# Kernel tuning notes

Hardware: AMD Instinct MI355X
Metric: run time of the kernel (lower is better)

Reference implementation:

```python
import jax, jax.numpy as jnp
import numpy as np

B, T, D = 256, 128, 64
H, A, O = 512, 128, 32


def setup_inputs() -> dict:
    key = jax.random.key(0)
    ks = jax.random.split(key, 16)
    u = lambda k, sh, lo, hi: jax.random.uniform(k, sh, jnp.float32, lo, hi)
    return {
        "x_states": jax.random.normal(ks[0], (B, T, D), jnp.float32),
        "x_dts": jax.random.uniform(ks[1], (B, T), jnp.float32) * 0.1,
        # StepwiseAttention params (stored [in, out])
        "Wq": u(ks[2], (D, A), -0.1, 0.1), "bq": u(ks[3], (A,), -0.1, 0.1),
        "Wk": u(ks[4], (H, A), -0.1, 0.1), "bk": u(ks[5], (A,), -0.1, 0.1),
        "Wv": u(ks[6], (H, A), -0.1, 0.1), "bv": u(ks[7], (A,), -0.1, 0.1),
        # LTCAttentionCell params
        "W_gd": u(ks[8], (D + H + A, 2 * H), -0.1, 0.1),
        "b_gd": u(ks[9], (2 * H,), -0.1, 0.1),
        "W_tau": u(ks[10], (H, H), -0.1, 0.1),
        "b_tau": u(ks[11], (H,), -0.1, 0.1),
        "gleak": u(ks[12], (H,), 0.001, 1.0),
        "cm": u(ks[13], (H,), 0.4, 0.6),
        # output head
        "W_fc": u(ks[14], (H, O), -0.1, 0.1),
        "b_fc": u(ks[15], (O,), -0.1, 0.1),
    }


def _forward(x_states, x_dts, Wq, bq, Wk, bk, Wv, bv,
             W_gd, b_gd, W_tau, b_tau, gleak, cm, W_fc, b_fc):
    scale = jnp.sqrt(jnp.asarray(A, jnp.float32))
    leak = jax.nn.softplus(cm) + jax.nn.softplus(gleak)  # [H]

    def dhdt(h, x_t, ctx):
        combined = jnp.concatenate([x_t, h, ctx], axis=1)        # [B, D+H+A]
        gd = combined @ W_gd + b_gd                              # [B, 2H]
        gate, dyn = jnp.split(gd, 2, axis=1)
        tau = jax.nn.softplus(h @ W_tau + b_tau)                 # [B, H]
        num = jax.nn.sigmoid(gate) * jnp.tanh(dyn) - h
        return num / (tau + leak + 1e-6)

    def step(carry, inp):
        h, hist = carry            # h [B,H], hist [B,T,H]
        t, x_t, dt = inp           # t scalar, x_t [B,D], dt [B]
        # stepwise attention over history h_1..h_t
        Q = x_t @ Wq + bq                                        # [B, A]
        K = hist @ Wk + bk                                       # [B, T, A]
        V = hist @ Wv + bv                                       # [B, T, A]
        scores = jnp.einsum('ba,bta->bt', Q, K) / scale          # [B, T]
        valid = jnp.arange(T) < t
        scores = jnp.where(valid[None, :], scores, -1e9)
        w = jax.nn.softmax(scores, axis=-1)
        ctx = jnp.einsum('bt,bta->ba', w, V)
        ctx = jnp.where(t > 0, ctx, jnp.zeros_like(ctx))         # empty history -> 0
        # one RK4 step (torchdiffeq 'rk4' = 3/8-rule variant), step size dt per sample
        dtc = dt[:, None]
        k1 = dhdt(h, x_t, ctx)
        k2 = dhdt(h + dtc * k1 / 3.0, x_t, ctx)
        k3 = dhdt(h + dtc * (k2 - k1 / 3.0), x_t, ctx)
        k4 = dhdt(h + dtc * (k1 - k2 + k3), x_t, ctx)
        h_next = h + dtc * (k1 + 3.0 * k2 + 3.0 * k3 + k4) / 8.0
        hist = jax.lax.dynamic_update_slice(hist, h_next[:, None, :], (0, t, 0))
        return (h_next, hist), None

    h0 = jnp.zeros((B, H), jnp.float32)
    hist0 = jnp.zeros((B, T, H), jnp.float32)
    xs = (jnp.arange(T), jnp.swapaxes(x_states, 0, 1), jnp.swapaxes(x_dts, 0, 1))
    (h_final, _), _ = jax.lax.scan(step, (h0, hist0), xs)
    return h_final @ W_fc + b_fc                                 # [B, O]


def reference(x_states, x_dts, Wq, bq, Wk, bk, Wv, bv,
              W_gd, b_gd, W_tau, b_tau, gleak, cm, W_fc, b_fc):
    return _forward(x_states, x_dts, Wq, bq, Wk, bk, Wv, bv,
                    W_gd, b_gd, W_tau, b_tau, gleak, cm, W_fc, b_fc)
```

## Files before the change

### kernel.cpp

```cpp
#include <hip/hip_runtime.h>
#include <math.h>

#define B_ 256
#define T_ 128
#define D_ 64
#define H_ 512
#define A_ 128
#define O_ 32

typedef __attribute__((ext_vector_type(8))) short short8;
typedef __attribute__((ext_vector_type(8))) unsigned short ushort8;
typedef __attribute__((ext_vector_type(4))) float floatx4;
typedef __attribute__((ext_vector_type(4))) unsigned int uintx4;
typedef unsigned long long ull;

__device__ __forceinline__ float sp_(float x) {
    return fmaxf(x, 0.f) + log1pf(expf(-fabsf(x)));
}
__device__ __forceinline__ float sigm_(float x) {
    return 1.f / (1.f + expf(-x));
}
__device__ __forceinline__ unsigned short f2bf_(float f) {
    unsigned int u = __float_as_uint(f);
    return (unsigned short)((u + 0x7FFFu + ((u >> 16) & 1u)) >> 16);
}
__device__ __forceinline__ float bf2f_(unsigned short u) {
    return __uint_as_float(((unsigned)u) << 16);
}

__device__ __forceinline__ void ld16sc(uintx4& d, const void* p) {
    asm volatile("global_load_dwordx4 %0, %1, off sc0 sc1"
                 : "=v"(d) : "v"(p) : "memory");
}
__device__ __forceinline__ void ld4sc(float& d, const void* p) {
    asm volatile("global_load_dword %0, %1, off sc0 sc1"
                 : "=v"(d) : "v"(p) : "memory");
}
__device__ __forceinline__ void vmwait4(uintx4& a, uintx4& b, uintx4& c,
                                        uintx4& d) {
    asm volatile("s_waitcnt vmcnt(0)"
                 : "+v"(a), "+v"(b), "+v"(c), "+v"(d)::"memory");
}
__device__ __forceinline__ void vmwait8(uintx4& a, uintx4& b, uintx4& c,
                                        uintx4& d, uintx4& e, uintx4& f,
                                        uintx4& g, uintx4& h) {
    asm volatile("s_waitcnt vmcnt(0)"
                 : "+v"(a), "+v"(b), "+v"(c), "+v"(d), "+v"(e), "+v"(f),
                   "+v"(g), "+v"(h)::"memory");
}
__device__ __forceinline__ void vmwait16f(float& a0, float& a1, float& a2,
                                          float& a3, float& a4, float& a5,
                                          float& a6, float& a7, float& b0,
                                          float& b1, float& b2, float& b3,
                                          float& b4, float& b5, float& b6,
                                          float& b7) {
    asm volatile("s_waitcnt vmcnt(0)"
                 : "+v"(a0), "+v"(a1), "+v"(a2), "+v"(a3), "+v"(a4), "+v"(a5),
                   "+v"(a6), "+v"(a7), "+v"(b0), "+v"(b1), "+v"(b2), "+v"(b3),
                   "+v"(b4), "+v"(b5), "+v"(b6), "+v"(b7)::"memory");
}
__device__ __forceinline__ floatx4 u2f_(uintx4 u) {
    union { uintx4 u; floatx4 f; } c;
    c.u = u;
    return c.f;
}

__device__ __forceinline__ void stf_(float* p, float v) {
    __hip_atomic_store(p, v, __ATOMIC_RELAXED, __HIP_MEMORY_SCOPE_SYSTEM);
}
__device__ __forceinline__ void st64_(ull* p, ull v) {
    __hip_atomic_store(p, v, __ATOMIC_RELAXED, __HIP_MEMORY_SCOPE_SYSTEM);
}

__global__ void init_kernel(unsigned short* __restrict__ hpack,
                            unsigned* __restrict__ bar) {
    int i = blockIdx.x * 256 + threadIdx.x;
    if (i < B_ * H_) hpack[i] = 0;
    if (i < 8192) bar[i] = 0u;
}

__global__ void pack_w_kernel(const float* __restrict__ W_gd,
                              const float* __restrict__ W_tau,
                              const float* __restrict__ Wk,
                              const float* __restrict__ Wv,
                              unsigned short* __restrict__ Wpack) {
    int gid = blockIdx.x * 256 + threadIdx.x;
    if (gid >= 1114112) return;
    int j = gid & 7;
    int l = (gid >> 3) & 63;
    int kpart = (l >> 4) * 8 + j;
    int npart = l & 15;
    float v;
    if (gid < 786432) {
        int f = gid >> 9;
        int s = f % 3;
        int rem = f / 3;
        int kb = rem & 15, ct = rem >> 4;
        int k = kb * 32 + kpart;
        int c = ct * 16 + npart;
        if (s == 0)      v = W_gd[(size_t)(D_ + k) * 1024 + c];
        else if (s == 1) v = W_gd[(size_t)(D_ + k) * 1024 + 512 + c];
        else             v = W_tau[(size_t)k * 512 + c];
    } else if (gid < 851968) {
        int r = gid - 786432;
        int f = r >> 9;
        int s = f & 1, kb = (f >> 1) & 1, ct = f >> 2;
        int k = kb * 32 + kpart;
        int c = ct * 16 + npart;
        v = W_gd[(size_t)k * 1024 + s * 512 + c];
    } else if (gid < 983040) {
        int r = gid - 851968;
        int f = r >> 9;
        int s = f & 1, kb = (f >> 1) & 3, ct = f >> 3;
        int k = kb * 32 + kpart;
        int c = ct * 16 + npart;
        v = W_gd[(size_t)(D_ + H_ + k) * 1024 + s * 512 + c];
    } else {
        int r = gid - 983040;
        int f = r >> 9;
        int kb = f & 15, c4 = f >> 4;
        int k = kb * 32 + kpart;
        int n = (c4 & 7) * 16 + npart;
        v = (c4 < 8) ? Wk[(size_t)k * A_ + n] : Wv[(size_t)k * A_ + n];
    }
    Wpack[gid] = f2bf_(v);
}

__device__ __forceinline__ void gsyncF(unsigned* flags, int j, unsigned cnt) {
    asm volatile("s_waitcnt vmcnt(0)" ::: "memory");
    __syncthreads();
    if (threadIdx.x == 0)
        __hip_atomic_store(flags + j * 64, cnt, __ATOMIC_RELAXED,
                           __HIP_MEMORY_SCOPE_SYSTEM);
    if (threadIdx.x < 8) {
        while (__hip_atomic_load(flags + threadIdx.x * 64, __ATOMIC_RELAXED,
                                 __HIP_MEMORY_SCOPE_SYSTEM) < cnt) {
            __builtin_amdgcn_s_sleep(1);
        }
    }
    __syncthreads();
}

struct P {
    const float *x, *dts, *Wq, *bq, *bk, *bv, *b_gd, *b_tau, *gleak, *cm,
        *W_fc, *b_fc;
    float *h, *ctx, *out, *Kpart, *Vpart;
    unsigned short* Kh;
    const unsigned short *Wy, *Wx, *Wc, *Wkv;
    unsigned short *hpack, *yapack, *ybpack;
    unsigned* bar;
};

__global__ __launch_bounds__(256, 1) void fused_kernel(P p) {
    const int tid = threadIdx.x;
    const int bid = blockIdx.x;
    const int lane = tid & 63;
    const int wave = tid >> 6;
    const int g = bid & 15;
    const int j = bid >> 4;
    const int ct = j * 4 + wave;
    unsigned* flags = p.bar + g * 512;
    unsigned cnt = 0;

    __shared__ float WqL[D_ * 129];
    __shared__ float xs4[2][D_];
    __shared__ float q4[2][A_];
    __shared__ float sc4[2][T_];
    __shared__ float red[2][2];
    __shared__ __align__(16) unsigned short AsL[32 * 256];
    __shared__ __align__(16) unsigned short ypbuf[4 * 256];
    __shared__ __align__(16) unsigned short As2[2 * 512];
    __shared__ unsigned short VhL[2][A_][136];

    const int quad = lane >> 4;
    const int c = ct * 16 + (lane & 15);
    const float btau = p.b_tau[c];
    const float lk = sp_(p.cm[c]) + sp_(p.gleak[c]) + 1e-6f;
    const float bgd_g = p.b_gd[c];
    const float bgd_d = p.b_gd[512 + c];
    const int aoff = (quad >> 1) * 256 + (lane & 15) * 16 + (quad & 1) * 8;
    const int ypw = wave * 256 + (lane & 15);

    const int sub = tid >> 7;
    const int tl = tid & 127;
    const int r = g * 16 + j * 2 + sub;
    const int rrow = r & 15;

    short8 wg[16], wd[16], wt[16];
    short8 wxg[2], wxd[2], wcg[4], wcd[4];
    {
        const short8* Wy8 = (const short8*)p.Wy;
        #pragma unroll
        for (int kb = 0; kb < 16; ++kb) {
            wg[kb] = Wy8[((ct * 16 + kb) * 3 + 0) * 64 + lane];
            wd[kb] = Wy8[((ct * 16 + kb) * 3 + 1) * 64 + lane];
            wt[kb] = Wy8[((ct * 16 + kb) * 3 + 2) * 64 + lane];
        }
        const short8* Wx8 = (const short8*)p.Wx;
        const short8* Wc8 = (const short8*)p.Wc;
        #pragma unroll
        for (int kb = 0; kb < 2; ++kb) {
            wxg[kb] = Wx8[((ct * 2 + kb) * 2 + 0) * 64 + lane];
            wxd[kb] = Wx8[((ct * 2 + kb) * 2 + 1) * 64 + lane];
        }
        #pragma unroll
        for (int kb = 0; kb < 4; ++kb) {
            wcg[kb] = Wc8[((ct * 4 + kb) * 2 + 0) * 64 + lane];
            wcd[kb] = Wc8[((ct * 4 + kb) * 2 + 1) * 64 + lane];
        }
    }

    for (int i = tid; i < D_ * A_; i += 256) {
        int d = i >> 7, a = i & 127;
        WqL[d * 129 + a] = p.Wq[i];
    }

    floatx4 hreg = {0.f, 0.f, 0.f, 0.f};
    floatx4 rk1, rk2, rk3, baseg, based, ycur, dt4;

    const short8* Wkv8 = (const short8*)p.Wkv;

    __syncthreads();

    for (int t = 0; t < T_; ++t) {
        {
            if (t > 0) {
                float kk[8], vv[8];
                #pragma unroll
                for (int jj = 0; jj < 8; ++jj) {
                    ld4sc(kk[jj],
                          p.Kpart + ((g * 8 + jj) * 16 + rrow) * 128 + tl);
                    ld4sc(vv[jj],
                          p.Vpart + ((g * 8 + jj) * 16 + rrow) * 128 + tl);
                }
                vmwait16f(kk[0], kk[1], kk[2], kk[3], kk[4], kk[5], kk[6],
                          kk[7], vv[0], vv[1], vv[2], vv[3], vv[4], vv[5],
                          vv[6], vv[7]);
                float ks = p.bk[tl], vs = p.bv[tl];
                #pragma unroll
                for (int jj = 0; jj < 8; ++jj) {
                    ks += kk[jj];
                    vs += vv[jj];
                }
                p.Kh[(size_t)(r * T_ + (t - 1)) * A_ + tl] = f2bf_(ks);
                VhL[sub][tl][t - 1] = f2bf_(vs);
            }
            if (tl < 16)
                ((float4*)xs4[sub])[tl] =
                    ((const float4*)&p.x[(r * T_ + t) * D_])[tl];
            __syncthreads();
            float qa = p.bq[tl];
            #pragma unroll 8
            for (int d = 0; d < D_; ++d) qa += xs4[sub][d] * WqL[d * 129 + tl];
            q4[sub][tl] = qa;
            __syncthreads();
            if (t == 0) {
                stf_(p.ctx + r * A_ + tl, 0.f);
            } else {
                const float rscale = 0.08838834764831845f;
                const int grp = tl >> 4, ln = tl & 15;
                float qv[8];
                #pragma unroll
                for (int i = 0; i < 8; ++i) qv[i] = q4[sub][ln * 8 + i];
                for (int s = grp; s < t; s += 8) {
                    ushort8 k8 = *((const ushort8*)(p.Kh +
                                     (size_t)(r * T_ + s) * A_) + ln);
                    float a2 = 0.f;
                    #pragma unroll
                    for (int i = 0; i < 8; ++i) a2 += bf2f_(k8[i]) * qv[i];
                    #pragma unroll
                    for (int off = 8; off > 0; off >>= 1)
                        a2 += __shfl_xor(a2, off, 16);
                    if (ln == 0) sc4[sub][s] = a2 * rscale;
                }
                __syncthreads();
                float mloc = -1e30f;
                for (int s = tl; s < t; s += 128) mloc = fmaxf(mloc, sc4[sub][s]);
                #pragma unroll
                for (int off = 32; off > 0; off >>= 1)
                    mloc = fmaxf(mloc, __shfl_xor(mloc, off, 64));
                if (lane == 0) red[sub][wave & 1] = mloc;
                __syncthreads();
                float m = fmaxf(red[sub][0], red[sub][1]);
                float ssum = 0.f;
                for (int s = tl; s < t; s += 128) {
                    float e = expf(sc4[sub][s] - m);
                    sc4[sub][s] = e;
                    ssum += e;
                }
                #pragma unroll
                for (int off = 32; off > 0; off >>= 1)
                    ssum += __shfl_xor(ssum, off, 64);
                __syncthreads();
                if (lane == 0) red[sub][wave & 1] = ssum;
                __syncthreads();
                float rs = 1.f / (red[sub][0] + red[sub][1]);
                const unsigned short* Vrow = &VhL[sub][tl][0];
                float ca0 = 0.f, ca1 = 0.f;
                int s0 = 0;
                for (; s0 + 16 <= t; s0 += 16) {
                    ushort8 v0 = *(const ushort8*)(Vrow + s0);
                    ushort8 v1 = *(const ushort8*)(Vrow + s0 + 8);
                    #pragma unroll
                    for (int i = 0; i < 8; ++i) {
                        ca0 += sc4[sub][s0 + i] * bf2f_(v0[i]);
                        ca1 += sc4[sub][s0 + 8 + i] * bf2f_(v1[i]);
                    }
                }
                if (s0 + 8 <= t) {
                    ushort8 v0 = *(const ushort8*)(Vrow + s0);
                    #pragma unroll
                    for (int i = 0; i < 8; ++i)
                        ca0 += sc4[sub][s0 + i] * bf2f_(v0[i]);
                    s0 += 8;
                }
                for (; s0 < t; ++s0) ca0 += sc4[sub][s0] * bf2f_(Vrow[s0]);
                stf_(p.ctx + r * A_ + tl, (ca0 + ca1) * rs);
            }
        }
        gsyncF(flags, j, ++cnt);

        {
            {
                const unsigned short* src = p.hpack + g * 8192;
                uintx4 av[4];
                #pragma unroll
                for (int i = 0; i < 4; ++i)
                    ld16sc(av[i], src + (size_t)tid * 8 + i * 2048);
                vmwait4(av[0], av[1], av[2], av[3]);
                #pragma unroll
                for (int i = 0; i < 4; ++i)
                    ((uintx4*)AsL)[tid + i * 256] = av[i];
            }
            const int mrow = lane & 15;
            const int kq = lane >> 4;
            const float* crow = &p.ctx[(g * 16 + mrow) * A_];
            uintx4 cc[8];
            #pragma unroll
            for (int kb = 0; kb < 4; ++kb) {
                ld16sc(cc[2 * kb], crow + kb * 32 + kq * 8);
                ld16sc(cc[2 * kb + 1], crow + kb * 32 + kq * 8 + 4);
            }
            vmwait8(cc[0], cc[1], cc[2], cc[3], cc[4], cc[5], cc[6], cc[7]);
            __syncthreads();

            #pragma unroll
            for (int i = 0; i < 4; ++i)
                dt4[i] = p.dts[(g * 16 + quad * 4 + i) * T_ + t];

            floatx4 bg = {0.f, 0.f, 0.f, 0.f};
            floatx4 bd = {0.f, 0.f, 0.f, 0.f};
            const float4* xrow =
                (const float4*)&p.x[((g * 16 + mrow) * T_ + t) * D_];
            #pragma unroll
            for (int kb = 0; kb < 2; ++kb) {
                float4 u = xrow[kb * 8 + kq * 2], v = xrow[kb * 8 + kq * 2 + 1];
                short8 ax;
                ax[0] = (short)f2bf_(u.x); ax[1] = (short)f2bf_(u.y);
                ax[2] = (short)f2bf_(u.z); ax[3] = (short)f2bf_(u.w);
                ax[4] = (short)f2bf_(v.x); ax[5] = (short)f2bf_(v.y);
                ax[6] = (short)f2bf_(v.z); ax[7] = (short)f2bf_(v.w);
                bg = __builtin_amdgcn_mfma_f32_16x16x32_bf16(ax, wxg[kb], bg, 0, 0, 0);
                bd = __builtin_amdgcn_mfma_f32_16x16x32_bf16(ax, wxd[kb], bd, 0, 0, 0);
            }
            #pragma unroll
            for (int kb = 0; kb < 4; ++kb) {
                floatx4 f0 = u2f_(cc[2 * kb]), f1 = u2f_(cc[2 * kb + 1]);
                short8 ac;
                ac[0] = (short)f2bf_(f0[0]); ac[1] = (short)f2bf_(f0[1]);
                ac[2] = (short)f2bf_(f0[2]); ac[3] = (short)f2bf_(f0[3]);
                ac[4] = (short)f2bf_(f1[0]); ac[5] = (short)f2bf_(f1[1]);
                ac[6] = (short)f2bf_(f1[2]); ac[7] = (short)f2bf_(f1[3]);
                bg = __builtin_amdgcn_mfma_f32_16x16x32_bf16(ac, wcg[kb], bg, 0, 0, 0);
                bd = __builtin_amdgcn_mfma_f32_16x16x32_bf16(ac, wcd[kb], bd, 0, 0, 0);
            }
            floatx4 ag = {0.f, 0.f, 0.f, 0.f};
            floatx4 ad = {0.f, 0.f, 0.f, 0.f};
            floatx4 at = {0.f, 0.f, 0.f, 0.f};
            #pragma unroll
            for (int kb = 0; kb < 16; ++kb) {
                short8 a = *(const short8*)(AsL + kb * 512 + aoff);
                ag = __builtin_amdgcn_mfma_f32_16x16x32_bf16(a, wg[kb], ag, 0, 0, 0);
                ad = __builtin_amdgcn_mfma_f32_16x16x32_bf16(a, wd[kb], ad, 0, 0, 0);
                at = __builtin_amdgcn_mfma_f32_16x16x32_bf16(a, wt[kb], at, 0, 0, 0);
            }
            #pragma unroll
            for (int i = 0; i < 4; ++i) {
                baseg[i] = bg[i] + bgd_g;
                based[i] = bd[i] + bgd_d;
                float gate = ag[i] + baseg[i];
                float dyn = ad[i] + based[i];
                float tau = sp_(at[i] + btau);
                float ki = (sigm_(gate) * tanhf(dyn) - hreg[i]) / (tau + lk);
                rk1[i] = ki;
                float yn = hreg[i] + dt4[i] * ki * (1.f / 3.f);
                ycur[i] = yn;
                ypbuf[ypw + (quad * 4 + i) * 16] = f2bf_(yn);
            }
            __syncthreads();
            st64_((ull*)p.yapack + g * 2048 + j * 256 + tid,
                  ((const ull*)ypbuf)[tid]);
        }
        gsyncF(flags, j, ++cnt);

        #pragma unroll 1
        for (int stage = 2; stage <= 4; ++stage) {
            const unsigned short* ysrc =
                (stage == 2) ? p.yapack : (stage == 3) ? p.ybpack : p.yapack;
            unsigned short* ydst =
                (stage == 2) ? p.ybpack : (stage == 3) ? p.yapack : p.hpack;
            {
                const unsigned short* src = ysrc + g * 8192;
                uintx4 av[4];
                #pragma unroll
                for (int i = 0; i < 4; ++i)
                    ld16sc(av[i], src + (size_t)tid * 8 + i * 2048);
                vmwait4(av[0], av[1], av[2], av[3]);
                #pragma unroll
                for (int i = 0; i < 4; ++i)
                    ((uintx4*)AsL)[tid + i * 256] = av[i];
            }
            __syncthreads();
            floatx4 ag = {0.f, 0.f, 0.f, 0.f};
            floatx4 ad = {0.f, 0.f, 0.f, 0.f};
            floatx4 at = {0.f, 0.f, 0.f, 0.f};
            #pragma unroll
            for (int kb = 0; kb < 16; ++kb) {
                short8 a = *(const short8*)(AsL + kb * 512 + aoff);
                ag = __builtin_amdgcn_mfma_f32_16x16x32_bf16(a, wg[kb], ag, 0, 0, 0);
                ad = __builtin_amdgcn_mfma_f32_16x16x32_bf16(a, wd[kb], ad, 0, 0, 0);
                at = __builtin_amdgcn_mfma_f32_16x16x32_bf16(a, wt[kb], at, 0, 0, 0);
            }
            const int lane_p = ((c >> 3) & 3) * 16;
            #pragma unroll
            for (int i = 0; i < 4; ++i) {
                float gate = ag[i] + baseg[i];
                float dyn = ad[i] + based[i];
                float tau = sp_(at[i] + btau);
                float ki = (sigm_(gate) * tanhf(dyn) - ycur[i]) / (tau + lk);
                float yn;
                if (stage == 2) {
                    rk2[i] = ki;
                    yn = hreg[i] + dt4[i] * (ki - rk1[i] * (1.f / 3.f));
                } else if (stage == 3) {
                    rk3[i] = ki;
                    yn = hreg[i] + dt4[i] * (rk1[i] - rk2[i] + ki);
                } else {
                    yn = hreg[i] +
                         dt4[i] * (rk1[i] + 3.f * rk2[i] + 3.f * rk3[i] + ki) * 0.125f;
                    hreg[i] = yn;
                }
                ycur[i] = yn;
                ypbuf[ypw + (quad * 4 + i) * 16] = f2bf_(yn);
                if (stage == 4)
                    As2[(wave >> 1) * 512 + (c & 7) +
                        (lane_p + quad * 4 + i) * 8] = f2bf_(yn);
            }
            __syncthreads();
            st64_((ull*)ydst + g * 2048 + j * 256 + tid,
                  ((const ull*)ypbuf)[tid]);
            if (stage == 4) {
                #pragma unroll
                for (int h4 = 0; h4 < 4; ++h4) {
                    const int c4 = wave + h4 * 4;
                    floatx4 acc = {0.f, 0.f, 0.f, 0.f};
                    #pragma unroll
                    for (int kk2 = 0; kk2 < 2; ++kk2) {
                        short8 a = *(const short8*)(As2 + (kk2 * 64 + lane) * 8);
                        acc = __builtin_amdgcn_mfma_f32_16x16x32_bf16(
                            a, Wkv8[(c4 * 16 + (j * 2 + kk2)) * 64 + lane], acc,
                            0, 0, 0);
                    }
                    const int ac = (c4 & 7) * 16 + (lane & 15);
                    float* part = (c4 < 8) ? p.Kpart : p.Vpart;
                    #pragma unroll
                    for (int i = 0; i < 4; ++i)
                        stf_(part + ((g * 8 + j) * 16 + quad * 4 + i) * 128 + ac,
                             acc[i]);
                }
            }
            gsyncF(flags, j, ++cnt);
        }
    }

    #pragma unroll
    for (int i = 0; i < 4; ++i)
        stf_(p.h + (g * 16 + quad * 4 + i) * H_ + c, hreg[i]);
    gsyncF(flags, j, ++cnt);
    {
        const int o = tl & 31, ks = tl >> 5;
        float acc = 0.f;
        const float* hrow = p.h + r * H_ + ks * 128;
        const float* wcol = p.W_fc + ks * 128 * O_ + o;
        #pragma unroll 1
        for (int rd = 0; rd < 4; ++rd) {
            uintx4 hh[8];
            #pragma unroll
            for (int i = 0; i < 8; ++i)
                ld16sc(hh[i], hrow + rd * 32 + i * 4);
            vmwait8(hh[0], hh[1], hh[2], hh[3], hh[4], hh[5], hh[6], hh[7]);
            #pragma unroll
            for (int i = 0; i < 8; ++i) {
                floatx4 f = u2f_(hh[i]);
                #pragma unroll
                for (int e = 0; e < 4; ++e)
                    acc += f[e] * wcol[(rd * 32 + i * 4 + e) * O_];
            }
        }
        sc4[sub][tl] = acc;
        __syncthreads();
        if (ks == 0)
            p.out[r * O_ + o] = acc + sc4[sub][o + 32] + sc4[sub][o + 64] +
                                sc4[sub][o + 96] + p.b_fc[o];
    }
}

extern "C" void kernel_launch(void* const* d_in, const int* in_sizes, int n_in,
                              void* d_out, int out_size, void* d_ws,
                              size_t ws_size, hipStream_t stream) {
    (void)in_sizes; (void)n_in; (void)out_size; (void)ws_size;
    P p;
    p.x = (const float*)d_in[0];
    p.dts = (const float*)d_in[1];
    p.Wq = (const float*)d_in[2];
    p.bq = (const float*)d_in[3];
    const float* Wk = (const float*)d_in[4];
    p.bk = (const float*)d_in[5];
    const float* Wv = (const float*)d_in[6];
    p.bv = (const float*)d_in[7];
    const float* W_gd = (const float*)d_in[8];
    p.b_gd = (const float*)d_in[9];
    const float* W_tau = (const float*)d_in[10];
    p.b_tau = (const float*)d_in[11];
    p.gleak = (const float*)d_in[12];
    p.cm = (const float*)d_in[13];
    p.W_fc = (const float*)d_in[14];
    p.b_fc = (const float*)d_in[15];
    p.out = (float*)d_out;

    float* ws = (float*)d_ws;
    p.h = ws;
    p.ctx = p.h + B_ * H_;
    p.Kpart = p.ctx + B_ * A_;
    p.Vpart = p.Kpart + 262144;
    unsigned short* Wpack = (unsigned short*)(p.Vpart + 262144);
    p.Wy = Wpack;
    p.Wx = Wpack + 786432;
    p.Wc = Wpack + 851968;
    p.Wkv = Wpack + 983040;
    p.hpack = Wpack + 1114112;
    p.yapack = p.hpack + B_ * H_;
    p.ybpack = p.yapack + B_ * H_;
    p.Kh = p.ybpack + B_ * H_;
    p.bar = (unsigned*)(p.Kh + (size_t)B_ * T_ * A_);

    init_kernel<<<512, 256, 0, stream>>>(p.hpack, p.bar);
    pack_w_kernel<<<4352, 256, 0, stream>>>(W_gd, W_tau, Wk, Wv, Wpack);

    fused_kernel<<<dim3(128), dim3(256), 0, stream>>>(p);
}
```

Measured before the change: 3.597 ms.

## Use XCC-local cache coherence for group sync when all blocks share an XCD

At kernel start, each of the eight blocks in a group reads its XCC_ID and runs a handshake to check whether all eight sit on the same XCD. If they do, the body is instantiated with global loads and stores that use only sc0, dropping system-scope sc1 coherence, so inter-block exchange of activations and flags can go through the shared L2 instead of farther out. Otherwise the original system-coherent path runs. This adds a startup handshake and doubles the code size. Correctness depends on the XCC detection and on the flag slots used for the handshake not colliding with the counters used later.

```diff
diff --git a/kernel.cpp b/kernel.cpp
--- a/kernel.cpp
+++ b/kernel.cpp
@@ -28,14 +28,65 @@
     return __uint_as_float(((unsigned)u) << 16);
 }
 
-__device__ __forceinline__ void ld16sc(uintx4& d, const void* p) {
-    asm volatile("global_load_dwordx4 %0, %1, off sc0 sc1"
-                 : "=v"(d) : "v"(p) : "memory");
-}
-__device__ __forceinline__ void ld4sc(float& d, const void* p) {
-    asm volatile("global_load_dword %0, %1, off sc0 sc1"
-                 : "=v"(d) : "v"(p) : "memory");
-}
+template <bool FAST>
+__device__ __forceinline__ void ld16x(uintx4& d, const void* p) {
+    if constexpr (FAST)
+        asm volatile("global_load_dwordx4 %0, %1, off sc0"
+                     : "=v"(d) : "v"(p) : "memory");
+    else
+        asm volatile("global_load_dwordx4 %0, %1, off sc0 sc1"
+                     : "=v"(d) : "v"(p) : "memory");
+}
+template <bool FAST>
+__device__ __forceinline__ void ld4x(float& d, const void* p) {
+    if constexpr (FAST)
+        asm volatile("global_load_dword %0, %1, off sc0"
+                     : "=v"(d) : "v"(p) : "memory");
+    else
+        asm volatile("global_load_dword %0, %1, off sc0 sc1"
+                     : "=v"(d) : "v"(p) : "memory");
+}
+template <bool FAST>
+__device__ __forceinline__ unsigned ldu32x(const unsigned* p) {
+    unsigned d;
+    if constexpr (FAST)
+        asm volatile("global_load_dword %0, %1, off sc0\n\t"
+                     "s_waitcnt vmcnt(0)"
+                     : "=v"(d) : "v"(p) : "memory");
+    else
+        asm volatile("global_load_dword %0, %1, off sc0 sc1\n\t"
+                     "s_waitcnt vmcnt(0)"
+                     : "=v"(d) : "v"(p) : "memory");
+    return d;
+}
+template <bool FAST>
+__device__ __forceinline__ void stfx(float* p, float v) {
+    if constexpr (FAST)
+        asm volatile("global_store_dword %0, %1, off sc0"
+                     :: "v"(p), "v"(v) : "memory");
+    else
+        asm volatile("global_store_dword %0, %1, off sc0 sc1"
+                     :: "v"(p), "v"(v) : "memory");
+}
+template <bool FAST>
+__device__ __forceinline__ void st64x(ull* p, ull v) {
+    if constexpr (FAST)
+        asm volatile("global_store_dwordx2 %0, %1, off sc0"
+                     :: "v"(p), "v"(v) : "memory");
+    else
+        asm volatile("global_store_dwordx2 %0, %1, off sc0 sc1"
+                     :: "v"(p), "v"(v) : "memory");
+}
+template <bool FAST>
+__device__ __forceinline__ void stu32x(unsigned* p, unsigned v) {
+    if constexpr (FAST)
+        asm volatile("global_store_dword %0, %1, off sc0"
+                     :: "v"(p), "v"(v) : "memory");
+    else
+        asm volatile("global_store_dword %0, %1, off sc0 sc1"
+                     :: "v"(p), "v"(v) : "memory");
+}
+
 __device__ __forceinline__ void vmwait4(uintx4& a, uintx4& b, uintx4& c,
                                         uintx4& d) {
     asm volatile("s_waitcnt vmcnt(0)"
@@ -63,13 +114,6 @@
     union { uintx4 u; floatx4 f; } c;
     c.u = u;
     return c.f;
-}
-
-__device__ __forceinline__ void stf_(float* p, float v) {
-    __hip_atomic_store(p, v, __ATOMIC_RELAXED, __HIP_MEMORY_SCOPE_SYSTEM);
-}
-__device__ __forceinline__ void st64_(ull* p, ull v) {
-    __hip_atomic_store(p, v, __ATOMIC_RELAXED, __HIP_MEMORY_SCOPE_SYSTEM);
 }
 
 __global__ void init_kernel(unsigned short* __restrict__ hpack,
@@ -126,15 +170,13 @@
     Wpack[gid] = f2bf_(v);
 }
 
-__device__ __forceinline__ void gsyncF(unsigned* flags, int j, unsigned cnt) {
+template <bool FAST>
+__device__ __forceinline__ void gsyncT(unsigned* flags, int j, unsigned cnt) {
     asm volatile("s_waitcnt vmcnt(0)" ::: "memory");
     __syncthreads();
-    if (threadIdx.x == 0)
-        __hip_atomic_store(flags + j * 64, cnt, __ATOMIC_RELAXED,
-                           __HIP_MEMORY_SCOPE_SYSTEM);
+    if (threadIdx.x == 0) stu32x<FAST>(flags + j * 64, cnt);
     if (threadIdx.x < 8) {
-        while (__hip_atomic_load(flags + threadIdx.x * 64, __ATOMIC_RELAXED,
-                                 __HIP_MEMORY_SCOPE_SYSTEM) < cnt) {
+        while (ldu32x<FAST>(flags + (int)threadIdx.x * 64) < cnt) {
             __builtin_amdgcn_s_sleep(1);
         }
     }
@@ -151,7 +193,21 @@
     unsigned* bar;
 };
 
-__global__ __launch_bounds__(256, 1) void fused_kernel(P p) {
+struct Shm {
+    float WqL[D_ * 129];
+    float xs4[2][D_];
+    float q4[2][A_];
+    float sc4[2][T_];
+    float red[2][2];
+    alignas(16) unsigned short AsL[32 * 256];
+    alignas(16) unsigned short ypbuf[4 * 256];
+    alignas(16) unsigned short As2[2 * 512];
+    unsigned short VhL[2][A_][136];
+    unsigned xcs[8];
+};
+
+template <bool FAST>
+__device__ __forceinline__ void run_body(const P& p, Shm& sh) {
     const int tid = threadIdx.x;
     const int bid = blockIdx.x;
     const int lane = tid & 63;
@@ -162,16 +218,6 @@
     unsigned* flags = p.bar + g * 512;
     unsigned cnt = 0;
 
-    __shared__ float WqL[D_ * 129];
-    __shared__ float xs4[2][D_];
-    __shared__ float q4[2][A_];
-    __shared__ float sc4[2][T_];
-    __shared__ float red[2][2];
-    __shared__ __align__(16) unsigned short AsL[32 * 256];
-    __shared__ __align__(16) unsigned short ypbuf[4 * 256];
-    __shared__ __align__(16) unsigned short As2[2 * 512];
-    __shared__ unsigned short VhL[2][A_][136];
-
     const int quad = lane >> 4;
     const int c = ct * 16 + (lane & 15);
     const float btau = p.b_tau[c];
@@ -212,7 +258,7 @@
 
     for (int i = tid; i < D_ * A_; i += 256) {
         int d = i >> 7, a = i & 127;
-        WqL[d * 129 + a] = p.Wq[i];
+        sh.WqL[d * 129 + a] = p.Wq[i];
     }
 
     floatx4 hreg = {0.f, 0.f, 0.f, 0.f};
@@ -228,10 +274,10 @@
                 float kk[8], vv[8];
                 #pragma unroll
                 for (int jj = 0; jj < 8; ++jj) {
-                    ld4sc(kk[jj],
-                          p.Kpart + ((g * 8 + jj) * 16 + rrow) * 128 + tl);
-                    ld4sc(vv[jj],
-                          p.Vpart + ((g * 8 + jj) * 16 + rrow) * 128 + tl);
+                    ld4x<FAST>(kk[jj],
+                               p.Kpart + ((g * 8 + jj) * 16 + rrow) * 128 + tl);
+                    ld4x<FAST>(vv[jj],
+                               p.Vpart + ((g * 8 + jj) * 16 + rrow) * 128 + tl);
                 }
                 vmwait16f(kk[0], kk[1], kk[2], kk[3], kk[4], kk[5], kk[6],
                           kk[7], vv[0], vv[1], vv[2], vv[3], vv[4], vv[5],
@@ -243,25 +289,26 @@
                     vs += vv[jj];
                 }
                 p.Kh[(size_t)(r * T_ + (t - 1)) * A_ + tl] = f2bf_(ks);
-                VhL[sub][tl][t - 1] = f2bf_(vs);
+                sh.VhL[sub][tl][t - 1] = f2bf_(vs);
             }
             if (tl < 16)
-                ((float4*)xs4[sub])[tl] =
+                ((float4*)sh.xs4[sub])[tl] =
                     ((const float4*)&p.x[(r * T_ + t) * D_])[tl];
             __syncthreads();
             float qa = p.bq[tl];
             #pragma unroll 8
-            for (int d = 0; d < D_; ++d) qa += xs4[sub][d] * WqL[d * 129 + tl];
-            q4[sub][tl] = qa;
+            for (int d = 0; d < D_; ++d)
+                qa += sh.xs4[sub][d] * sh.WqL[d * 129 + tl];
+            sh.q4[sub][tl] = qa;
             __syncthreads();
             if (t == 0) {
-                stf_(p.ctx + r * A_ + tl, 0.f);
+                stfx<FAST>(p.ctx + r * A_ + tl, 0.f);
             } else {
                 const float rscale = 0.08838834764831845f;
                 const int grp = tl >> 4, ln = tl & 15;
                 float qv[8];
                 #pragma unroll
-                for (int i = 0; i < 8; ++i) qv[i] = q4[sub][ln * 8 + i];
+                for (int i = 0; i < 8; ++i) qv[i] = sh.q4[sub][ln * 8 + i];
                 for (int s = grp; s < t; s += 8) {
                     ushort8 k8 = *((const ushort8*)(p.Kh +
                                      (size_t)(r * T_ + s) * A_) + ln);
@@ -271,31 +318,32 @@
                     #pragma unroll
                     for (int off = 8; off > 0; off >>= 1)
                         a2 += __shfl_xor(a2, off, 16);
-                    if (ln == 0) sc4[sub][s] = a2 * rscale;
+                    if (ln == 0) sh.sc4[sub][s] = a2 * rscale;
                 }
                 __syncthreads();
                 float mloc = -1e30f;
-                for (int s = tl; s < t; s += 128) mloc = fmaxf(mloc, sc4[sub][s]);
+                for (int s = tl; s < t; s += 128)
+                    mloc = fmaxf(mloc, sh.sc4[sub][s]);
                 #pragma unroll
                 for (int off = 32; off > 0; off >>= 1)
                     mloc = fmaxf(mloc, __shfl_xor(mloc, off, 64));
-                if (lane == 0) red[sub][wave & 1] = mloc;
+                if (lane == 0) sh.red[sub][wave & 1] = mloc;
                 __syncthreads();
-                float m = fmaxf(red[sub][0], red[sub][1]);
+                float m = fmaxf(sh.red[sub][0], sh.red[sub][1]);
                 float ssum = 0.f;
                 for (int s = tl; s < t; s += 128) {
-                    float e = expf(sc4[sub][s] - m);
-                    sc4[sub][s] = e;
+                    float e = expf(sh.sc4[sub][s] - m);
+                    sh.sc4[sub][s] = e;
                     ssum += e;
                 }
                 #pragma unroll
                 for (int off = 32; off > 0; off >>= 1)
                     ssum += __shfl_xor(ssum, off, 64);
                 __syncthreads();
-                if (lane == 0) red[sub][wave & 1] = ssum;
+                if (lane == 0) sh.red[sub][wave & 1] = ssum;
                 __syncthreads();
-                float rs = 1.f / (red[sub][0] + red[sub][1]);
-                const unsigned short* Vrow = &VhL[sub][tl][0];
+                float rs = 1.f / (sh.red[sub][0] + sh.red[sub][1]);
+                const unsigned short* Vrow = &sh.VhL[sub][tl][0];
                 float ca0 = 0.f, ca1 = 0.f;
                 int s0 = 0;
                 for (; s0 + 16 <= t; s0 += 16) {
@@ -303,22 +351,22 @@
                     ushort8 v1 = *(const ushort8*)(Vrow + s0 + 8);
                     #pragma unroll
                     for (int i = 0; i < 8; ++i) {
-                        ca0 += sc4[sub][s0 + i] * bf2f_(v0[i]);
-                        ca1 += sc4[sub][s0 + 8 + i] * bf2f_(v1[i]);
+                        ca0 += sh.sc4[sub][s0 + i] * bf2f_(v0[i]);
+                        ca1 += sh.sc4[sub][s0 + 8 + i] * bf2f_(v1[i]);
                     }
                 }
                 if (s0 + 8 <= t) {
                     ushort8 v0 = *(const ushort8*)(Vrow + s0);
                     #pragma unroll
                     for (int i = 0; i < 8; ++i)
-                        ca0 += sc4[sub][s0 + i] * bf2f_(v0[i]);
+                        ca0 += sh.sc4[sub][s0 + i] * bf2f_(v0[i]);
                     s0 += 8;
                 }
-                for (; s0 < t; ++s0) ca0 += sc4[sub][s0] * bf2f_(Vrow[s0]);
-                stf_(p.ctx + r * A_ + tl, (ca0 + ca1) * rs);
-            }
-        }
-        gsyncF(flags, j, ++cnt);
+                for (; s0 < t; ++s0) ca0 += sh.sc4[sub][s0] * bf2f_(Vrow[s0]);
+                stfx<FAST>(p.ctx + r * A_ + tl, (ca0 + ca1) * rs);
+            }
+        }
+        gsyncT<FAST>(flags, j, ++cnt);
 
         {
             {
@@ -326,11 +374,11 @@
                 uintx4 av[4];
                 #pragma unroll
                 for (int i = 0; i < 4; ++i)
-                    ld16sc(av[i], src + (size_t)tid * 8 + i * 2048);
+                    ld16x<FAST>(av[i], src + (size_t)tid * 8 + i * 2048);
                 vmwait4(av[0], av[1], av[2], av[3]);
                 #pragma unroll
                 for (int i = 0; i < 4; ++i)
-                    ((uintx4*)AsL)[tid + i * 256] = av[i];
+                    ((uintx4*)sh.AsL)[tid + i * 256] = av[i];
             }
             const int mrow = lane & 15;
             const int kq = lane >> 4;
@@ -338,8 +386,8 @@
             uintx4 cc[8];
             #pragma unroll
             for (int kb = 0; kb < 4; ++kb) {
-                ld16sc(cc[2 * kb], crow + kb * 32 + kq * 8);
-                ld16sc(cc[2 * kb + 1], crow + kb * 32 + kq * 8 + 4);
+                ld16x<FAST>(cc[2 * kb], crow + kb * 32 + kq * 8);
+                ld16x<FAST>(cc[2 * kb + 1], crow + kb * 32 + kq * 8 + 4);
             }
             vmwait8(cc[0], cc[1], cc[2], cc[3], cc[4], cc[5], cc[6], cc[7]);
             __syncthreads();
@@ -379,7 +427,7 @@
             floatx4 at = {0.f, 0.f, 0.f, 0.f};
             #pragma unroll
             for (int kb = 0; kb < 16; ++kb) {
-                short8 a = *(const short8*)(AsL + kb * 512 + aoff);
+                short8 a = *(const short8*)(sh.AsL + kb * 512 + aoff);
                 ag = __builtin_amdgcn_mfma_f32_16x16x32_bf16(a, wg[kb], ag, 0, 0, 0);
                 ad = __builtin_amdgcn_mfma_f32_16x16x32_bf16(a, wd[kb], ad, 0, 0, 0);
                 at = __builtin_amdgcn_mfma_f32_16x16x32_bf16(a, wt[kb], at, 0, 0, 0);
@@ -395,13 +443,13 @@
                 rk1[i] = ki;
                 float yn = hreg[i] + dt4[i] * ki * (1.f / 3.f);
                 ycur[i] = yn;
-                ypbuf[ypw + (quad * 4 + i) * 16] = f2bf_(yn);
+                sh.ypbuf[ypw + (quad * 4 + i) * 16] = f2bf_(yn);
             }
             __syncthreads();
-            st64_((ull*)p.yapack + g * 2048 + j * 256 + tid,
-                  ((const ull*)ypbuf)[tid]);
-        }
-        gsyncF(flags, j, ++cnt);
+            st64x<FAST>((ull*)p.yapack + g * 2048 + j * 256 + tid,
+                        ((const ull*)sh.ypbuf)[tid]);
+        }
+        gsyncT<FAST>(flags, j, ++cnt);
 
         #pragma unroll 1
         for (int stage = 2; stage <= 4; ++stage) {
@@ -414,11 +462,11 @@
                 uintx4 av[4];
                 #pragma unroll
                 for (int i = 0; i < 4; ++i)
-                    ld16sc(av[i], src + (size_t)tid * 8 + i * 2048);
+                    ld16x<FAST>(av[i], src + (size_t)tid * 8 + i * 2048);
                 vmwait4(av[0], av[1], av[2], av[3]);
                 #pragma unroll
                 for (int i = 0; i < 4; ++i)
-                    ((uintx4*)AsL)[tid + i * 256] = av[i];
+                    ((uintx4*)sh.AsL)[tid + i * 256] = av[i];
             }
             __syncthreads();
             floatx4 ag = {0.f, 0.f, 0.f, 0.f};
@@ -426,7 +474,7 @@
             floatx4 at = {0.f, 0.f, 0.f, 0.f};
             #pragma unroll
             for (int kb = 0; kb < 16; ++kb) {
-                short8 a = *(const short8*)(AsL + kb * 512 + aoff);
+                short8 a = *(const short8*)(sh.AsL + kb * 512 + aoff);
                 ag = __builtin_amdgcn_mfma_f32_16x16x32_bf16(a, wg[kb], ag, 0, 0, 0);
                 ad = __builtin_amdgcn_mfma_f32_16x16x32_bf16(a, wd[kb], ad, 0, 0, 0);
                 at = __builtin_amdgcn_mfma_f32_16x16x32_bf16(a, wt[kb], at, 0, 0, 0);
@@ -451,14 +499,14 @@
                     hreg[i] = yn;
                 }
                 ycur[i] = yn;
-                ypbuf[ypw + (quad * 4 + i) * 16] = f2bf_(yn);
+                sh.ypbuf[ypw + (quad * 4 + i) * 16] = f2bf_(yn);
                 if (stage == 4)
-                    As2[(wave >> 1) * 512 + (c & 7) +
-                        (lane_p + quad * 4 + i) * 8] = f2bf_(yn);
+                    sh.As2[(wave >> 1) * 512 + (c & 7) +
+                           (lane_p + quad * 4 + i) * 8] = f2bf_(yn);
             }
             __syncthreads();
-            st64_((ull*)ydst + g * 2048 + j * 256 + tid,
-                  ((const ull*)ypbuf)[tid]);
+            st64x<FAST>((ull*)ydst + g * 2048 + j * 256 + tid,
+                        ((const ull*)sh.ypbuf)[tid]);
             if (stage == 4) {
                 #pragma unroll
                 for (int h4 = 0; h4 < 4; ++h4) {
@@ -466,7 +514,7 @@
                     floatx4 acc = {0.f, 0.f, 0.f, 0.f};
                     #pragma unroll
                     for (int kk2 = 0; kk2 < 2; ++kk2) {
-                        short8 a = *(const short8*)(As2 + (kk2 * 64 + lane) * 8);
+                        short8 a = *(const short8*)(sh.As2 + (kk2 * 64 + lane) * 8);
                         acc = __builtin_amdgcn_mfma_f32_16x16x32_bf16(
                             a, Wkv8[(c4 * 16 + (j * 2 + kk2)) * 64 + lane], acc,
                             0, 0, 0);
@@ -475,18 +523,20 @@
                     float* part = (c4 < 8) ? p.Kpart : p.Vpart;
                     #pragma unroll
                     for (int i = 0; i < 4; ++i)
-                        stf_(part + ((g * 8 + j) * 16 + quad * 4 + i) * 128 + ac,
-                             acc[i]);
-                }
-            }
-            gsyncF(flags, j, ++cnt);
+                        stfx<FAST>(part +
+                                       ((g * 8 + j) * 16 + quad * 4 + i) * 128 +
+                                       ac,
+                                   acc[i]);
+                }
+            }
+            gsyncT<FAST>(flags, j, ++cnt);
         }
     }
 
     #pragma unroll
     for (int i = 0; i < 4; ++i)
-        stf_(p.h + (g * 16 + quad * 4 + i) * H_ + c, hreg[i]);
-    gsyncF(flags, j, ++cnt);
+        stfx<FAST>(p.h + (g * 16 + quad * 4 + i) * H_ + c, hreg[i]);
+    gsyncT<FAST>(flags, j, ++cnt);
     {
         const int o = tl & 31, ks = tl >> 5;
         float acc = 0.f;
@@ -497,7 +547,7 @@
             uintx4 hh[8];
             #pragma unroll
             for (int i = 0; i < 8; ++i)
-                ld16sc(hh[i], hrow + rd * 32 + i * 4);
+                ld16x<FAST>(hh[i], hrow + rd * 32 + i * 4);
             vmwait8(hh[0], hh[1], hh[2], hh[3], hh[4], hh[5], hh[6], hh[7]);
             #pragma unroll
             for (int i = 0; i < 8; ++i) {
@@ -507,12 +557,76 @@
                     acc += f[e] * wcol[(rd * 32 + i * 4 + e) * O_];
             }
         }
-        sc4[sub][tl] = acc;
+        sh.sc4[sub][tl] = acc;
         __syncthreads();
         if (ks == 0)
-            p.out[r * O_ + o] = acc + sc4[sub][o + 32] + sc4[sub][o + 64] +
-                                sc4[sub][o + 96] + p.b_fc[o];
-    }
+            p.out[r * O_ + o] = acc + sh.sc4[sub][o + 32] + sh.sc4[sub][o + 64] +
+                                sh.sc4[sub][o + 96] + p.b_fc[o];
+    }
+}
+
+__global__ __launch_bounds__(256, 1) void fused_kernel(P p) {
+    __shared__ Shm sh;
+    const int tid = threadIdx.x;
+    const int bid = blockIdx.x;
+    const int g = bid & 15;
+    const int j = bid >> 4;
+    unsigned* flags = p.bar + g * 512;
+
+    unsigned myxcc;
+    asm volatile("s_getreg_b32 %0, hwreg(HW_REG_XCC_ID)" : "=s"(myxcc));
+    myxcc = (myxcc & 15u) + 1u;
+    if (tid == 0) stu32x<true>(flags + j * 64 + 32, myxcc);
+    if (tid < 8) {
+        unsigned v = 0;
+        for (int it = 0; it < 8192; ++it) {
+            v = ldu32x<true>(flags + tid * 64 + 32);
+            if (v) break;
+            __builtin_amdgcn_s_sleep(2);
+        }
+        sh.xcs[tid] = (v == myxcc) ? 1u : 0u;
+    }
+    __syncthreads();
+    bool ok8 = true;
+    #pragma unroll
+    for (int i = 0; i < 8; ++i) ok8 = ok8 && (sh.xcs[i] != 0u);
+    __syncthreads();
+
+    bool trial_ok = false;
+    if (ok8) {
+        if (tid == 0) stu32x<true>(flags + j * 64 + 33, 1u);
+        if (tid < 8) {
+            unsigned v = 0;
+            for (int it = 0; it < 8192; ++it) {
+                v = ldu32x<true>(flags + tid * 64 + 33);
+                if (v) break;
+                __builtin_amdgcn_s_sleep(2);
+            }
+            sh.xcs[tid] = v ? 1u : 0u;
+        }
+        __syncthreads();
+        trial_ok = true;
+        #pragma unroll
+        for (int i = 0; i < 8; ++i) trial_ok = trial_ok && (sh.xcs[i] != 0u);
+        __syncthreads();
+    }
+
+    if (tid == 0) stu32x<false>(flags + j * 64 + 1, trial_ok ? 2u : 1u);
+    if (tid < 8) {
+        unsigned v;
+        while ((v = ldu32x<false>(flags + tid * 64 + 1)) == 0u)
+            __builtin_amdgcn_s_sleep(1);
+        sh.xcs[tid] = (v == 2u) ? 1u : 0u;
+    }
+    __syncthreads();
+    bool same8 = true;
+    #pragma unroll
+    for (int i = 0; i < 8; ++i) same8 = same8 && (sh.xcs[i] != 0u);
+
+    if (same8)
+        run_body<true>(p, sh);
+    else
+        run_body<false>(p, sh);
 }
 
 extern "C" void kernel_launch(void* const* d_in, const int* in_sizes, int n_in,
```

New measurement: 4.497 ms. +25.0%, slower.

## Prefetch h state early, store RK stage outputs directly, drop staging syncs

Applied to the files above, without the earlier changes.

The packed h state, dt values and x row loads move to the start of each timestep so they overlap with the K/V reduction and attention work. The h-dependent MFMA chain now runs before waiting on the ctx loads, which hides that load latency. Each RK stage result is written straight to global memory as a 16-bit store instead of being staged through LDS with a barrier and a 64-bit store, removing a block sync per stage. In exchange it issues many small scattered stores, and it relies on the grid sync ordering the early hpack load after the previous step's writes.

```diff
diff --git a/kernel.cpp b/kernel.cpp
--- a/kernel.cpp
+++ b/kernel.cpp
@@ -35,6 +35,10 @@
 __device__ __forceinline__ void ld4sc(float& d, const void* p) {
     asm volatile("global_load_dword %0, %1, off sc0 sc1"
                  : "=v"(d) : "v"(p) : "memory");
+}
+__device__ __forceinline__ void st16sc(unsigned short* p, unsigned v) {
+    asm volatile("global_store_short %0, %1, off sc0 sc1"
+                 :: "v"(p), "v"(v) : "memory");
 }
 __device__ __forceinline__ void vmwait4(uintx4& a, uintx4& b, uintx4& c,
                                         uintx4& d) {
@@ -66,9 +70,6 @@
 }
 
 __device__ __forceinline__ void stf_(float* p, float v) {
-    __hip_atomic_store(p, v, __ATOMIC_RELAXED, __HIP_MEMORY_SCOPE_SYSTEM);
-}
-__device__ __forceinline__ void st64_(ull* p, ull v) {
     __hip_atomic_store(p, v, __ATOMIC_RELAXED, __HIP_MEMORY_SCOPE_SYSTEM);
 }
 
@@ -168,7 +169,6 @@
     __shared__ float sc4[2][T_];
     __shared__ float red[2][2];
     __shared__ __align__(16) unsigned short AsL[32 * 256];
-    __shared__ __align__(16) unsigned short ypbuf[4 * 256];
     __shared__ __align__(16) unsigned short As2[2 * 512];
     __shared__ unsigned short VhL[2][A_][136];
 
@@ -179,7 +179,7 @@
     const float bgd_g = p.b_gd[c];
     const float bgd_d = p.b_gd[512 + c];
     const int aoff = (quad >> 1) * 256 + (lane & 15) * 16 + (quad & 1) * 8;
-    const int ypw = wave * 256 + (lane & 15);
+    const int ybase = g * 8192 + j * 1024 + wave * 256 + (lane & 15);
 
     const int sub = tid >> 7;
     const int tl = tid & 127;
@@ -223,7 +223,27 @@
     __syncthreads();
 
     for (int t = 0; t < T_; ++t) {
+        float4 xr[4];
         {
+            uintx4 av[4];
+            {
+                const unsigned short* src = p.hpack + g * 8192;
+                #pragma unroll
+                for (int i = 0; i < 4; ++i)
+                    ld16sc(av[i], src + (size_t)tid * 8 + i * 2048);
+            }
+            #pragma unroll
+            for (int i = 0; i < 4; ++i)
+                dt4[i] = p.dts[(g * 16 + quad * 4 + i) * T_ + t];
+            {
+                const float4* xrow =
+                    (const float4*)&p.x[((g * 16 + (lane & 15)) * T_ + t) * D_];
+                #pragma unroll
+                for (int kb = 0; kb < 2; ++kb) {
+                    xr[2 * kb] = xrow[kb * 8 + quad * 2];
+                    xr[2 * kb + 1] = xrow[kb * 8 + quad * 2 + 1];
+                }
+            }
             if (t > 0) {
                 float kk[8], vv[8];
                 #pragma unroll
@@ -245,6 +265,11 @@
                 p.Kh[(size_t)(r * T_ + (t - 1)) * A_ + tl] = f2bf_(ks);
                 VhL[sub][tl][t - 1] = f2bf_(vs);
             }
+            vmwait4(av[0], av[1], av[2], av[3]);
+            #pragma unroll
+            for (int i = 0; i < 4; ++i)
+                ((uintx4*)AsL)[tid + i * 256] = av[i];
+
             if (tl < 16)
                 ((float4*)xs4[sub])[tl] =
                     ((const float4*)&p.x[(r * T_ + t) * D_])[tl];
@@ -321,40 +346,20 @@
         gsyncF(flags, j, ++cnt);
 
         {
-            {
-                const unsigned short* src = p.hpack + g * 8192;
-                uintx4 av[4];
-                #pragma unroll
-                for (int i = 0; i < 4; ++i)
-                    ld16sc(av[i], src + (size_t)tid * 8 + i * 2048);
-                vmwait4(av[0], av[1], av[2], av[3]);
-                #pragma unroll
-                for (int i = 0; i < 4; ++i)
-                    ((uintx4*)AsL)[tid + i * 256] = av[i];
-            }
             const int mrow = lane & 15;
-            const int kq = lane >> 4;
             const float* crow = &p.ctx[(g * 16 + mrow) * A_];
             uintx4 cc[8];
             #pragma unroll
             for (int kb = 0; kb < 4; ++kb) {
-                ld16sc(cc[2 * kb], crow + kb * 32 + kq * 8);
-                ld16sc(cc[2 * kb + 1], crow + kb * 32 + kq * 8 + 4);
-            }
-            vmwait8(cc[0], cc[1], cc[2], cc[3], cc[4], cc[5], cc[6], cc[7]);
-            __syncthreads();
-
-            #pragma unroll
-            for (int i = 0; i < 4; ++i)
-                dt4[i] = p.dts[(g * 16 + quad * 4 + i) * T_ + t];
+                ld16sc(cc[2 * kb], crow + kb * 32 + quad * 8);
+                ld16sc(cc[2 * kb + 1], crow + kb * 32 + quad * 8 + 4);
+            }
 
             floatx4 bg = {0.f, 0.f, 0.f, 0.f};
             floatx4 bd = {0.f, 0.f, 0.f, 0.f};
-            const float4* xrow =
-                (const float4*)&p.x[((g * 16 + mrow) * T_ + t) * D_];
             #pragma unroll
             for (int kb = 0; kb < 2; ++kb) {
-                float4 u = xrow[kb * 8 + kq * 2], v = xrow[kb * 8 + kq * 2 + 1];
+                float4 u = xr[2 * kb], v = xr[2 * kb + 1];
                 short8 ax;
                 ax[0] = (short)f2bf_(u.x); ax[1] = (short)f2bf_(u.y);
                 ax[2] = (short)f2bf_(u.z); ax[3] = (short)f2bf_(u.w);
@@ -363,6 +368,17 @@
                 bg = __builtin_amdgcn_mfma_f32_16x16x32_bf16(ax, wxg[kb], bg, 0, 0, 0);
                 bd = __builtin_amdgcn_mfma_f32_16x16x32_bf16(ax, wxd[kb], bd, 0, 0, 0);
             }
+            floatx4 ag = {0.f, 0.f, 0.f, 0.f};
+            floatx4 ad = {0.f, 0.f, 0.f, 0.f};
+            floatx4 at = {0.f, 0.f, 0.f, 0.f};
+            #pragma unroll
+            for (int kb = 0; kb < 16; ++kb) {
+                short8 a = *(const short8*)(AsL + kb * 512 + aoff);
+                ag = __builtin_amdgcn_mfma_f32_16x16x32_bf16(a, wg[kb], ag, 0, 0, 0);
+                ad = __builtin_amdgcn_mfma_f32_16x16x32_bf16(a, wd[kb], ad, 0, 0, 0);
+                at = __builtin_amdgcn_mfma_f32_16x16x32_bf16(a, wt[kb], at, 0, 0, 0);
+            }
+            vmwait8(cc[0], cc[1], cc[2], cc[3], cc[4], cc[5], cc[6], cc[7]);
             #pragma unroll
             for (int kb = 0; kb < 4; ++kb) {
                 floatx4 f0 = u2f_(cc[2 * kb]), f1 = u2f_(cc[2 * kb + 1]);
@@ -373,16 +389,6 @@
                 ac[6] = (short)f2bf_(f1[2]); ac[7] = (short)f2bf_(f1[3]);
                 bg = __builtin_amdgcn_mfma_f32_16x16x32_bf16(ac, wcg[kb], bg, 0, 0, 0);
                 bd = __builtin_amdgcn_mfma_f32_16x16x32_bf16(ac, wcd[kb], bd, 0, 0, 0);
-            }
-            floatx4 ag = {0.f, 0.f, 0.f, 0.f};
-            floatx4 ad = {0.f, 0.f, 0.f, 0.f};
-            floatx4 at = {0.f, 0.f, 0.f, 0.f};
-            #pragma unroll
-            for (int kb = 0; kb < 16; ++kb) {
-                short8 a = *(const short8*)(AsL + kb * 512 + aoff);
-                ag = __builtin_amdgcn_mfma_f32_16x16x32_bf16(a, wg[kb], ag, 0, 0, 0);
-                ad = __builtin_amdgcn_mfma_f32_16x16x32_bf16(a, wd[kb], ad, 0, 0, 0);
-                at = __builtin_amdgcn_mfma_f32_16x16x32_bf16(a, wt[kb], at, 0, 0, 0);
             }
             #pragma unroll
             for (int i = 0; i < 4; ++i) {
@@ -395,11 +401,9 @@
                 rk1[i] = ki;
                 float yn = hreg[i] + dt4[i] * ki * (1.f / 3.f);
                 ycur[i] = yn;
-                ypbuf[ypw + (quad * 4 + i) * 16] = f2bf_(yn);
-            }
-            __syncthreads();
-            st64_((ull*)p.yapack + g * 2048 + j * 256 + tid,
-                  ((const ull*)ypbuf)[tid]);
+                st16sc(p.yapack + ybase + (quad * 4 + i) * 16,
+                       (unsigned)f2bf_(yn));
+            }
         }
         gsyncF(flags, j, ++cnt);
 
@@ -451,15 +455,14 @@
                     hreg[i] = yn;
                 }
                 ycur[i] = yn;
-                ypbuf[ypw + (quad * 4 + i) * 16] = f2bf_(yn);
+                st16sc(ydst + ybase + (quad * 4 + i) * 16,
+                       (unsigned)f2bf_(yn));
                 if (stage == 4)
                     As2[(wave >> 1) * 512 + (c & 7) +
                         (lane_p + quad * 4 + i) * 8] = f2bf_(yn);
             }
-            __syncthreads();
-            st64_((ull*)ydst + g * 2048 + j * 256 + tid,
-                  ((const ull*)ypbuf)[tid]);
             if (stage == 4) {
+                __syncthreads();
                 #pragma unroll
                 for (int h4 = 0; h4 < 4; ++h4) {
                     const int c4 = wave + h4 * 4;
```

Result: no change. 3.635 ms (+1.0%).
